# Optimization experiments

Hardware: AMD Instinct MI355X
Metric: run time of the kernel (lower is better)

Reference implementation:

```python
import jax, jax.numpy as jnp
import numpy as np

B_, L_, O_, N_, S_, U_, DEL, HID, K = 16, 128, 128, 256, 64, 32, 64, 512, 4
D_OUT = DEL + N_ * U_ + N_ * S_  # 24640


def setup_inputs() -> dict:
    key = jax.random.key(0)
    ks = jax.random.split(key, 12)
    return {
        "x": jax.random.normal(ks[0], (B_, O_ + L_, S_), jnp.float32),
        "u": jax.random.normal(ks[1], (B_, 2 * L_, U_), jnp.float32),
        "A": jax.random.normal(ks[2], (N_, 1), jnp.float32) / 20.0,
        "W0": jax.random.normal(ks[3], (HID, S_), jnp.float32) * 0.05,
        "b0": jnp.zeros((HID,), jnp.float32),
        "W1": jax.random.normal(ks[4], (N_, HID), jnp.float32) * 0.05,
        "b1": jnp.zeros((N_,), jnp.float32),
        "conv_w": jax.random.normal(ks[5], (N_ + U_, 1, K), jnp.float32) * 0.3,
        "conv_b": jnp.zeros((N_ + U_,), jnp.float32),
        "Wg": jax.random.normal(ks[6], (D_OUT, N_ + U_), jnp.float32) * 0.05,
        "bg": jnp.zeros((D_OUT,), jnp.float32),
        "Wdt": jax.random.normal(ks[7], (N_, DEL), jnp.float32) * 0.05,
        "bdt": jnp.zeros((N_,), jnp.float32),
    }


def reference(x, u, A, W0, b0, W1, b1, conv_w, conv_b, Wg, bg, Wdt, bdt):
    def proj_x(v):  # Linear -> relu -> Linear (project_x)
        return jax.nn.relu(v @ W0.T + b0) @ W1.T + b1

    u = u[:, :, :U_]
    z0 = proj_x(x[:, O_ - 1, :])                       # (B, N)

    # ---- generate_matrices ----
    x_all = proj_x(x[:, :O_ - 1, :])                   # (B, O-1, N)
    u_all = u[:, :O_ - 1, :]                           # (B, O-1, U)
    old = jax.nn.silu(jnp.concatenate([x_all, u_all], axis=2))  # (B, O-1, N+U)
    old = jnp.transpose(old, (0, 2, 1))                # (B, N+U, O-1)
    old = jax.lax.conv_general_dilated(
        old, conv_w, window_strides=(1,), padding=[(K - 1, K - 1)],
        dimension_numbers=("NCH", "OIH", "NCH"), feature_group_count=N_ + U_,
    ) + conv_b[None, :, None]
    old = old[:, :, -L_:]                              # last L timesteps
    old = jax.nn.silu(jnp.transpose(old, (0, 2, 1)))   # (B, L, N+U)
    gen = old @ Wg.T + bg                              # (B, L, delta + N*U + N*S)
    delta, Bm, Cm = jnp.split(gen, [DEL, DEL + N_ * U_], axis=-1)
    delta = jax.nn.softplus(delta @ Wdt.T + bdt)       # (B, L, N)
    Bm = Bm.reshape(B_, L_, N_, U_)
    Cm = Cm.reshape(B_, L_, N_, S_)

    # ---- discretion_matrices ----
    a = A[:, 0]
    a = -jnp.where(a > 0, a, jnp.expm1(a))             # -celu(A), alpha=1
    dA = jnp.exp(delta * a)                            # (B, L, N)
    dB = ((dA - 1.0) * (1.0 / a))[..., None] * Bm      # (B, L, N, U)

    # ---- selective_scan ----
    u0 = u[:, O_ - 1:O_ - 1 + L_, :]                   # (B, L, U)
    xt = x[:, O_:O_ + L_, :]                           # (B, L, S) targets

    def step(z, inp):
        dAi, dBi, ui, Ci, xti = inp
        z = z * dAi + jnp.einsum("bnu,bu->bn", dBi, ui)
        y = jnp.einsum("bns,bn->bs", Ci, z)
        return z, (y, jnp.mean((y - xti) ** 2))

    xs = (
        jnp.swapaxes(dA, 0, 1), jnp.swapaxes(dB, 0, 1),
        jnp.swapaxes(u0, 0, 1), jnp.swapaxes(Cm, 0, 1), jnp.swapaxes(xt, 0, 1),
    )
    _, (ys, ls) = jax.lax.scan(step, z0, xs)
    loss = jnp.sum(ls) / L_
    return loss, jax.lax.stop_gradient(ys)             # ys: (L, B, S), detached as in torch
```

## Files before the change

kernel.cpp:

```cpp
#include <hip/hip_runtime.h>
#include <math.h>

#define B_   16
#define L_   128
#define O_   128
#define N_   256
#define S_   64
#define U_   32
#define DEL_ 64
#define HID_ 512
#define CH_  288
#define M_   2048
#define KD_  288
#define CM_BASE (DEL_ + N_*U_)
#define NSLICE 32

typedef __bf16 bf16_t;
typedef bf16_t bf16x8 __attribute__((ext_vector_type(8)));
typedef float  f32x4  __attribute__((ext_vector_type(4)));

#define AS1(p) ((const __attribute__((address_space(1))) void*)(unsigned long long)(const void*)(p))
#define AS3(p) ((__attribute__((address_space(3))) void*)(unsigned int)(unsigned long long)(const void*)(p))

__device__ __forceinline__ float silu_f(float x){ return x / (1.f + expf(-x)); }
__device__ __forceinline__ float softplus_f(float x){
  return fmaxf(x, 0.f) + log1pf(expf(-fabsf(x)));
}

__device__ __forceinline__ void cvt8(const float* src, bf16_t* dst){
  float4 a = ((const float4*)src)[0];
  float4 b = ((const float4*)src)[1];
  bf16x8 o;
  o[0]=(bf16_t)a.x; o[1]=(bf16_t)a.y; o[2]=(bf16_t)a.z; o[3]=(bf16_t)a.w;
  o[4]=(bf16_t)b.x; o[5]=(bf16_t)b.y; o[6]=(bf16_t)b.z; o[7]=(bf16_t)b.w;
  *(bf16x8*)dst = o;
}

#define CVT_BLOCKS 3465
#define W0_BLOCKS  16
#define W1_BLOCKS  64
#define XB_BLOCKS  64
__global__ void k_prep(const float* __restrict__ Wg, bf16_t* __restrict__ Wgbf,
                       const float* __restrict__ W0, bf16_t* __restrict__ W0bf,
                       const float* __restrict__ W1, bf16_t* __restrict__ W1bf,
                       const float* __restrict__ x,  bf16_t* __restrict__ xbf,
                       float* __restrict__ lossa){
  if (blockIdx.x == 0 && threadIdx.x < 2) lossa[threadIdx.x] = 0.f;
  if (blockIdx.x < CVT_BLOCKS) {
    int i = blockIdx.x*256 + threadIdx.x;
    if (i >= 887040) return;
    cvt8(Wg + (size_t)i*8, Wgbf + (size_t)i*8);
  } else if (blockIdx.x < CVT_BLOCKS + W0_BLOCKS) {
    int i = (blockIdx.x - CVT_BLOCKS)*256 + threadIdx.x;
    if (i >= 4096) return;
    cvt8(W0 + (size_t)i*8, W0bf + (size_t)i*8);
  } else if (blockIdx.x < CVT_BLOCKS + W0_BLOCKS + W1_BLOCKS) {
    int i = (blockIdx.x - CVT_BLOCKS - W0_BLOCKS)*256 + threadIdx.x;
    if (i >= 16384) return;
    cvt8(W1 + (size_t)i*8, W1bf + (size_t)i*8);
  } else {
    int i = (blockIdx.x - CVT_BLOCKS - W0_BLOCKS - W1_BLOCKS)*256 + threadIdx.x;
    if (i >= 16384) return;
    int m = i >> 3, c0 = (i & 7)*8;
    int b = m >> 7, t = m & 127;
    cvt8(x + (size_t)(((b<<8)+t)<<6) + c0, xbf + (size_t)m*64 + c0);
  }
}

#define STAGE64(GBASE, ROW0G, STRIDE, LDSARR)                                        \
  { const bf16_t* gp = (GBASE) + (size_t)((ROW0G) + wave*16 + lm)*(STRIDE) + kk + lq*8; \
    __builtin_amdgcn_global_load_lds(AS1(gp), AS3(&(LDSARR)[wave*512]), 16, 0, 0); }

__global__ __launch_bounds__(256) void k_mlp1m(
    const bf16_t* __restrict__ xbf, const bf16_t* __restrict__ W0bf,
    const float* __restrict__ b0, bf16_t* __restrict__ Hbf){
  __shared__ __align__(16) bf16_t As[64*32];
  __shared__ __align__(16) bf16_t Bs[64*32];
  int tid = threadIdx.x;
  int wave = tid >> 6, lane = tid & 63;
  int wm = wave & 1, wn = wave >> 1;
  int nt = blockIdx.x, mt = blockIdx.y;
  int m0 = mt*64, n0 = nt*64;
  int lm = lane & 15, lq = lane >> 4;

  f32x4 acc[2][2];
  #pragma unroll
  for (int i=0;i<2;i++)
    #pragma unroll
    for (int j=0;j<2;j++){ acc[i][j][0]=0.f;acc[i][j][1]=0.f;acc[i][j][2]=0.f;acc[i][j][3]=0.f; }

  #pragma unroll
  for (int kk = 0; kk < 64; kk += 32) {
    STAGE64(xbf, m0, 64, As);
    STAGE64(W0bf, n0, 64, Bs);
    __syncthreads();
    bf16x8 af[2], bff[2];
    #pragma unroll
    for (int i=0;i<2;i++) af[i]  = *(const bf16x8*)&As[(wm*2 + i)*512 + lane*8];
    #pragma unroll
    for (int j=0;j<2;j++) bff[j] = *(const bf16x8*)&Bs[(wn*2 + j)*512 + lane*8];
    #pragma unroll
    for (int i=0;i<2;i++)
      #pragma unroll
      for (int j=0;j<2;j++)
        acc[i][j] = __builtin_amdgcn_mfma_f32_16x16x32_bf16(af[i], bff[j], acc[i][j], 0,0,0);
    __syncthreads();
  }
  #pragma unroll
  for (int i=0;i<2;i++)
    #pragma unroll
    for (int j=0;j<2;j++){
      int col = n0 + wn*32 + j*16 + lm;
      float bb = b0[col];
      #pragma unroll
      for (int r=0;r<4;r++){
        int row = m0 + wm*32 + i*16 + lq*4 + r;
        Hbf[(size_t)row*HID_ + col] = (bf16_t)fmaxf(acc[i][j][r] + bb, 0.f);
      }
    }
}

__global__ __launch_bounds__(256) void k_mlp2m(
    const bf16_t* __restrict__ Hbf, const bf16_t* __restrict__ W1bf,
    const float* __restrict__ b1, float* __restrict__ P){
  __shared__ __align__(16) bf16_t As[64*32];
  __shared__ __align__(16) bf16_t Bs[64*32];
  int tid = threadIdx.x;
  int wave = tid >> 6, lane = tid & 63;
  int wm = wave & 1, wn = wave >> 1;
  int nt = blockIdx.x, mt = blockIdx.y;
  int m0 = mt*64, n0 = nt*64;
  int lm = lane & 15, lq = lane >> 4;

  f32x4 acc[2][2];
  #pragma unroll
  for (int i=0;i<2;i++)
    #pragma unroll
    for (int j=0;j<2;j++){ acc[i][j][0]=0.f;acc[i][j][1]=0.f;acc[i][j][2]=0.f;acc[i][j][3]=0.f; }

  for (int kk = 0; kk < HID_; kk += 32) {
    STAGE64(Hbf, m0, HID_, As);
    STAGE64(W1bf, n0, HID_, Bs);
    __syncthreads();
    bf16x8 af[2], bff[2];
    #pragma unroll
    for (int i=0;i<2;i++) af[i]  = *(const bf16x8*)&As[(wm*2 + i)*512 + lane*8];
    #pragma unroll
    for (int j=0;j<2;j++) bff[j] = *(const bf16x8*)&Bs[(wn*2 + j)*512 + lane*8];
    #pragma unroll
    for (int i=0;i<2;i++)
      #pragma unroll
      for (int j=0;j<2;j++)
        acc[i][j] = __builtin_amdgcn_mfma_f32_16x16x32_bf16(af[i], bff[j], acc[i][j], 0,0,0);
    __syncthreads();
  }
  #pragma unroll
  for (int i=0;i<2;i++)
    #pragma unroll
    for (int j=0;j<2;j++){
      int col = n0 + wn*32 + j*16 + lm;
      float bb = b1[col];
      #pragma unroll
      for (int r=0;r<4;r++){
        int row = m0 + wm*32 + i*16 + lq*4 + r;
        P[(size_t)row*N_ + col] = acc[i][j][r] + bb;
      }
    }
}

__global__ __launch_bounds__(256) void k_convdelta(
    const float* __restrict__ P, const float* __restrict__ u,
    const float* __restrict__ cw, const float* __restrict__ cb,
    const float* __restrict__ Wg, const float* __restrict__ bg,
    const float* __restrict__ Wdt, const float* __restrict__ bdt,
    const float* __restrict__ Ap, bf16_t* __restrict__ oldbf,
    float* __restrict__ dA, float* __restrict__ coef){
  __shared__ __align__(16) float olds[4*KD_];
  __shared__ float dr[4][64];
  int tid = threadIdx.x;
  int m0 = blockIdx.x * 4;
  int b = m0 >> 7, l0 = m0 & 127;
  for (int e = tid; e < 4*CH_; e += 256) {
    int r = e / CH_, c = e - r*CH_;
    int l = l0 + r;
    float acc = cb[c];
    #pragma unroll
    for (int k = 0; k < 4; k++) {
      int t = l + k - 1;
      if (t >= 0 && t <= O_-2) {
        float s = (c < N_) ? P[((b<<7)+t)*N_ + c] : u[((b<<8)+t)*U_ + (c-N_)];
        acc += silu_f(s) * cw[c*4 + k];
      }
    }
    float v = silu_f(acc);
    olds[e] = v;
    oldbf[(size_t)(m0+r)*CH_ + c] = (bf16_t)v;
  }
  __syncthreads();
  {
    int d = tid & 63;
    int r = tid >> 6;
    const float* wrow = Wg + (size_t)d*KD_;
    const float* orow = olds + r*KD_;
    float s = 0.f;
    for (int k = 0; k < KD_; k++) s += orow[k] * wrow[k];
    dr[r][d] = s + bg[d];
  }
  __syncthreads();
  int n = tid;
  float wrow[64];
  #pragma unroll
  for (int d = 0; d < 64; d++) wrow[d] = Wdt[n*64 + d];
  float a0 = Ap[n];
  float a = -(a0 > 0.f ? a0 : expm1f(a0));
  float inva = 1.f / a;
  float bd = bdt[n];
  #pragma unroll
  for (int r = 0; r < 4; r++) {
    float s = bd;
    #pragma unroll
    for (int d = 0; d < 64; d++) s += dr[r][d] * wrow[d];
    float dd = softplus_f(s);
    float e  = expf(dd * a);
    size_t m = m0 + r;
    dA[m*N_ + n]   = e;
    coef[m*N_ + n] = (e - 1.f) * inva;
  }
}

#define STAGE_FR96(GBASE, ROW0G, LDSARR)                                                 \
  { _Pragma("unroll")                                                                    \
    for (int c = 0; c < 3; c++) {                                                        \
      _Pragma("unroll")                                                                  \
      for (int q = 0; q < 2; q++) {                                                      \
        int g = wave*2 + q;                                                              \
        const bf16_t* gp = (GBASE) + (size_t)((ROW0G) + g*16 + lm)*KD_ + kk + c*32 + lq*8;\
        __builtin_amdgcn_global_load_lds(AS1(gp), AS3(&(LDSARR)[c*4096 + g*512]), 16, 0, 0);\
      } } }

__global__ __launch_bounds__(256, 2) void k_bmfma(
    const bf16_t* __restrict__ oldbf, const bf16_t* __restrict__ Wgbf,
    const float* __restrict__ bg, const float* __restrict__ u,
    const float* __restrict__ coef, const float* __restrict__ dAg,
    const float* __restrict__ Pg, float* __restrict__ zall){
  __shared__ union {
    struct { __align__(16) bf16_t A[3*4096]; __align__(16) bf16_t B[3*4096]; } st;
    struct { float wl[128][4]; float dal[128][4]; } sc;
  } sm;
  int tid = threadIdx.x;
  int wave = tid >> 6, lane = tid & 63;
  int wm = wave & 1, wn = wave >> 1;
  int mt = blockIdx.y, nt = blockIdx.x;
  int m0 = mt*128, ncol0 = nt*128;
  int lm = lane & 15, lq = lane >> 4;

  f32x4 acc[4][4];
  #pragma unroll
  for (int i=0;i<4;i++)
    #pragma unroll
    for (int j=0;j<4;j++){ acc[i][j][0]=0.f;acc[i][j][1]=0.f;acc[i][j][2]=0.f;acc[i][j][3]=0.f; }

  for (int kk = 0; kk < KD_; kk += 96) {
    STAGE_FR96(oldbf, m0, sm.st.A);
    STAGE_FR96(Wgbf, DEL_ + ncol0, sm.st.B);
    __syncthreads();
    for (int c = 0; c < 3; c++) {
      bf16x8 af[4], bff[4];
      #pragma unroll
      for (int i=0;i<4;i++) af[i]  = *(const bf16x8*)&sm.st.A[c*4096 + (wm*4 + i)*512 + lane*8];
      #pragma unroll
      for (int j=0;j<4;j++) bff[j] = *(const bf16x8*)&sm.st.B[c*4096 + (wn*4 + j)*512 + lane*8];
      #pragma unroll
      for (int i=0;i<4;i++)
        #pragma unroll
        for (int j=0;j<4;j++)
          acc[i][j] = __builtin_amdgcn_mfma_f32_16x16x32_bf16(af[i], bff[j], acc[i][j], 0,0,0);
    }
    __syncthreads();
  }

  for (int e = tid; e < 512; e += 256)
    sm.sc.dal[e>>2][e&3] = dAg[(size_t)(m0 + (e>>2))*N_ + nt*4 + (e&3)];

  float bgv[4];
  #pragma unroll
  for (int j=0;j<4;j++) bgv[j] = bg[DEL_ + ncol0 + wn*64 + j*16 + lm];
  float p[2][4][4];
  #pragma unroll
  for (int a=0;a<2;a++)
    #pragma unroll
    for (int i=0;i<4;i++)
      #pragma unroll
      for (int r=0;r<4;r++) p[a][i][r]=0.f;
  #pragma unroll
  for (int i=0;i<4;i++){
    #pragma unroll
    for (int r=0;r<4;r++){
      int m = m0 + wm*64 + i*16 + lq*4 + r;
      int b = m >> 7, l = m & 127;
      const float* urow = u + ((size_t)(b<<8) + 127 + l)*U_;
      #pragma unroll
      for (int j=0;j<4;j++){
        float uu = urow[(j&1)*16 + lm];
        p[j>>1][i][r] += (acc[i][j][r] + bgv[j]) * uu;
      }
    }
  }
  #pragma unroll
  for (int mk = 1; mk < 16; mk <<= 1){
    #pragma unroll
    for (int a=0;a<2;a++)
      #pragma unroll
      for (int i=0;i<4;i++)
        #pragma unroll
        for (int r=0;r<4;r++) p[a][i][r] += __shfl_xor(p[a][i][r], mk);
  }
  if (lm == 0){
    #pragma unroll
    for (int nl=0;nl<2;nl++){
      int n = ((ncol0 + wn*64 + nl*32) >> 5);
      int nc = wn*2 + nl;
      #pragma unroll
      for (int i=0;i<4;i++)
        #pragma unroll
        for (int r=0;r<4;r++){
          int l = wm*64 + i*16 + lq*4 + r;
          sm.sc.wl[l][nc] = coef[(size_t)(m0+l)*N_ + n] * p[nl][i][r];
        }
    }
  }
  __syncthreads();

  {
    int nc = wave;
    int n = nt*4 + nc;
    float z0 = Pg[(size_t)(m0 + 127)*N_ + n];
    int l0 = lane*2;
    float a0 = sm.sc.dal[l0][nc],   w0 = sm.sc.wl[l0][nc];
    float a1 = sm.sc.dal[l0+1][nc], w1 = sm.sc.wl[l0+1][nc];
    float A = a0*a1, Bv = w0*a1 + w1;
    #pragma unroll
    for (int d = 1; d < 64; d <<= 1){
      float Ap = __shfl_up(A, d);
      float Bp = __shfl_up(Bv, d);
      if (lane >= d){ Bv = Bp*A + Bv; A = Ap*A; }
    }
    float Ae = __shfl_up(A, 1);
    float Be = __shfl_up(Bv, 1);
    if (lane == 0){ Ae = 1.f; Be = 0.f; }
    float zp = z0*Ae + Be;
    float za = zp*a0 + w0;
    float zb = za*a1 + w1;
    zall[(size_t)(m0 + l0)*N_ + n]     = za;
    zall[(size_t)(m0 + l0 + 1)*N_ + n] = zb;
  }
}

__global__ __launch_bounds__(256, 2) void k_cmfma(
    const bf16_t* __restrict__ oldbf, const bf16_t* __restrict__ Wgbf,
    const float* __restrict__ bg, const float* __restrict__ zall,
    float* __restrict__ ypart){
  __shared__ union {
    struct { __align__(16) bf16_t A[3*4096];
             __align__(16) bf16_t Bb[3*4096];
             float zl[128][8]; } st;
    float ylds[128][64];
  } sm;
  int tid = threadIdx.x;
  int wave = tid >> 6, lane = tid & 63;
  int wm = wave & 1, wn = wave >> 1;
  int mt = blockIdx.y, grp = blockIdx.x;
  int m0 = mt*128;
  int lm = lane & 15, lq = lane >> 4;

  for (int e = tid; e < 1024; e += 256)
    sm.st.zl[e>>3][e&7] = zall[(size_t)(m0 + (e>>3))*N_ + grp*8 + (e&7)];

  f32x4 yacc[4][4];
  #pragma unroll
  for (int i=0;i<4;i++)
    #pragma unroll
    for (int j=0;j<4;j++){ yacc[i][j][0]=0.f;yacc[i][j][1]=0.f;yacc[i][j][2]=0.f;yacc[i][j][3]=0.f; }

  for (int kh = 0; kh < 3; kh++) {
    int kk = kh*96;
    STAGE_FR96(oldbf, m0, sm.st.A);
    for (int it = 0; it < 4; it++) {
      int ncol0 = (grp*4 + it)*128;
      STAGE_FR96(Wgbf, CM_BASE + ncol0, sm.st.Bb);
      __syncthreads();
      f32x4 acc[4][4];
      #pragma unroll
      for (int i=0;i<4;i++)
        #pragma unroll
        for (int j=0;j<4;j++){ acc[i][j][0]=0.f;acc[i][j][1]=0.f;acc[i][j][2]=0.f;acc[i][j][3]=0.f; }
      for (int c = 0; c < 3; c++) {
        bf16x8 af[4], bff[4];
        #pragma unroll
        for (int i=0;i<4;i++) af[i]  = *(const bf16x8*)&sm.st.A[c*4096 + (wm*4 + i)*512 + lane*8];
        #pragma unroll
        for (int j=0;j<4;j++) bff[j] = *(const bf16x8*)&sm.st.Bb[c*4096 + (wn*4 + j)*512 + lane*8];
        #pragma unroll
        for (int i=0;i<4;i++)
          #pragma unroll
          for (int j=0;j<4;j++)
            acc[i][j] = __builtin_amdgcn_mfma_f32_16x16x32_bf16(af[i], bff[j], acc[i][j], 0,0,0);
      }
      int nl = it*2 + wn;
      float bgv[4];
      #pragma unroll
      for (int j=0;j<4;j++)
        bgv[j] = (kh == 2) ? bg[CM_BASE + ncol0 + wn*64 + j*16 + lm] : 0.f;
      #pragma unroll
      for (int i=0;i<4;i++){
        #pragma unroll
        for (int r=0;r<4;r++){
          float zv = sm.st.zl[wm*64 + i*16 + lq*4 + r][nl];
          #pragma unroll
          for (int j=0;j<4;j++)
            yacc[i][j][r] += (acc[i][j][r] + bgv[j]) * zv;
        }
      }
      __syncthreads();
    }
  }

  if (wn == 1){
    #pragma unroll
    for (int i=0;i<4;i++)
      #pragma unroll
      for (int j=0;j<4;j++)
        #pragma unroll
        for (int r=0;r<4;r++){
          int ml = wm*64 + i*16 + lq*4 + r;
          sm.ylds[ml][j*16 + lm] = yacc[i][j][r];
        }
  }
  __syncthreads();
  if (wn == 0){
    float* dst = ypart + (size_t)grp*(M_*S_);
    #pragma unroll
    for (int i=0;i<4;i++)
      #pragma unroll
      for (int j=0;j<4;j++)
        #pragma unroll
        for (int r=0;r<4;r++){
          int ml = wm*64 + i*16 + lq*4 + r;
          int s = j*16 + lm;
          dst[(size_t)(m0+ml)*S_ + s] = yacc[i][j][r] + sm.ylds[ml][s];
        }
  }
}

__global__ void k_finalize(const float* __restrict__ ypart, const float* __restrict__ x,
                           float* __restrict__ out, float* __restrict__ lossacc){
  __shared__ float red[256];
  int tid = threadIdx.x;
  float ls = 0.f;
  #pragma unroll
  for (int q = 0; q < 2; q++) {
    int e = blockIdx.x*512 + q*256 + tid;
    int m = e >> 6, s = e & 63;
    int b = m >> 7, l = m & 127;
    float yv = 0.f;
    #pragma unroll 8
    for (int g = 0; g < NSLICE; g++) yv += ypart[(size_t)g*(M_*S_) + e];
    out[1 + (size_t)((l<<4) + b)*S_ + s] = yv;
    float xv = x[((size_t)(b<<8) + 128 + l)*S_ + s];
    float d = yv - xv;
    ls += d*d;
  }
  red[tid] = ls; __syncthreads();
  for (int st = 128; st > 0; st >>= 1) {
    if (tid < st) red[tid] += red[tid+st];
    __syncthreads();
  }
  if (tid == 0) {
    atomicAdd(&lossacc[0], red[0]);
    __threadfence();
    unsigned old = atomicAdd((unsigned*)&lossacc[1], 1u);
    if (old == 255u) {
      float tot = atomicAdd(&lossacc[0], 0.f);
      out[0] = tot * (1.f / (float)(B_*S_*L_));
    }
  }
}

extern "C" void kernel_launch(void* const* d_in, const int* in_sizes, int n_in,
                              void* d_out, int out_size, void* d_ws, size_t ws_size,
                              hipStream_t stream) {
  const float* x   = (const float*)d_in[0];
  const float* u   = (const float*)d_in[1];
  const float* Ap  = (const float*)d_in[2];
  const float* W0  = (const float*)d_in[3];
  const float* b0  = (const float*)d_in[4];
  const float* W1  = (const float*)d_in[5];
  const float* b1  = (const float*)d_in[6];
  const float* cw  = (const float*)d_in[7];
  const float* cb  = (const float*)d_in[8];
  const float* Wg  = (const float*)d_in[9];
  const float* bg  = (const float*)d_in[10];
  const float* Wdt = (const float*)d_in[11];
  const float* bdt = (const float*)d_in[12];
  float* out = (float*)d_out;

  float* ws    = (float*)d_ws;
  float* zall  = ws;
  float* lossa = zall + 524288;
  bf16_t* oldbf = (bf16_t*)(lossa + 512);
  bf16_t* Wgbf  = (bf16_t*)(lossa + 512 + 294912);
  bf16_t* W0bf  = (bf16_t*)(lossa + 512 + 294912 + 3548160);
  bf16_t* W1bf  = (bf16_t*)(lossa + 512 + 294912 + 3548160 + 16384);
  bf16_t* xbf   = (bf16_t*)(lossa + 512 + 294912 + 3548160 + 16384 + 65536);
  bf16_t* Hbf   = (bf16_t*)(lossa + 512 + 294912 + 3548160 + 16384 + 65536 + 65536);
  float* R     = lossa + 512 + 294912 + 3548160 + 16384 + 65536 + 65536 + 524288;
  float* Pp    = R;
  float* dA    = Pp   + 524288;
  float* coef  = dA   + 524288;
  float* ypart = R;

  k_prep<<<CVT_BLOCKS + W0_BLOCKS + W1_BLOCKS + XB_BLOCKS, 256, 0, stream>>>(
      Wg, Wgbf, W0, W0bf, W1, W1bf, x, xbf, lossa);
  k_mlp1m<<<dim3(HID_/64, M_/64), 256, 0, stream>>>(xbf, W0bf, b0, Hbf);
  k_mlp2m<<<dim3(N_/64, M_/64), 256, 0, stream>>>(Hbf, W1bf, b1, Pp);
  k_convdelta<<<M_/4, 256, 0, stream>>>(Pp, u, cw, cb, Wg, bg, Wdt, bdt, Ap,
                                        oldbf, dA, coef);
  k_bmfma<<<dim3(64, 16), 256, 0, stream>>>(oldbf, Wgbf, bg, u, coef, dA, Pp, zall);
  k_cmfma<<<dim3(32, 16), 256, 0, stream>>>(oldbf, Wgbf, bg, zall, ypart);
  k_finalize<<<256, 256, 0, stream>>>(ypart, x, out, lossa);
}
```

Before: 208.7 us.

## Double-buffer LDS staging in MLP, B-matrix and C-matrix GEMM kernels

Converts the four MFMA GEMM kernels from single-buffered load-sync-compute loops to double-buffered LDS pipelines. The next K-slice or weight tile is issued with global_load_lds while the current one feeds the MFMAs. The goal is to hide global-memory latency behind compute and drop one barrier per iteration. It doubles the B tile buffer in k_cmfma and changes k_bmfma to 32-wide K steps, which raises LDS use and may lower occupancy or add iterations. Correctness relies on the async LDS loads finishing before the single barrier per step, which waits only on counters the compiler inserts.

```diff
diff --git a/kernel.cpp b/kernel.cpp
--- a/kernel.cpp
+++ b/kernel.cpp
@@ -67,15 +67,33 @@
   }
 }
 
-#define STAGE64(GBASE, ROW0G, STRIDE, LDSARR)                                        \
-  { const bf16_t* gp = (GBASE) + (size_t)((ROW0G) + wave*16 + lm)*(STRIDE) + kk + lq*8; \
-    __builtin_amdgcn_global_load_lds(AS1(gp), AS3(&(LDSARR)[wave*512]), 16, 0, 0); }
+#define STAGE64K(GBASE, ROW0G, STRIDE, KK, LDSP)                                     \
+  { const bf16_t* gp_ = (GBASE) + (size_t)((ROW0G) + wave*16 + lm)*(STRIDE) + (KK) + lq*8; \
+    __builtin_amdgcn_global_load_lds(AS1(gp_), AS3((LDSP) + wave*512), 16, 0, 0); }
+
+#define STAGE32(GBASE, ROW0G, KK, LDSP)                                              \
+  { _Pragma("unroll")                                                                \
+    for (int l_ = 0; l_ < 2; l_++) {                                                 \
+      int g_ = wave*2 + l_;                                                          \
+      const bf16_t* gp_ = (GBASE) + (size_t)((ROW0G) + g_*16 + lm)*KD_ + (KK) + lq*8;\
+      __builtin_amdgcn_global_load_lds(AS1(gp_), AS3((LDSP) + g_*512), 16, 0, 0);    \
+    } }
+
+#define STAGE_FR96(GBASE, ROW0G, KK, LDSP)                                           \
+  { _Pragma("unroll")                                                                \
+    for (int c_ = 0; c_ < 3; c_++) {                                                 \
+      _Pragma("unroll")                                                              \
+      for (int q_ = 0; q_ < 2; q_++) {                                               \
+        int g_ = wave*2 + q_;                                                        \
+        const bf16_t* gp_ = (GBASE) + (size_t)((ROW0G) + g_*16 + lm)*KD_ + (KK) + c_*32 + lq*8;\
+        __builtin_amdgcn_global_load_lds(AS1(gp_), AS3((LDSP) + c_*4096 + g_*512), 16, 0, 0);\
+      } } }
 
 __global__ __launch_bounds__(256) void k_mlp1m(
     const bf16_t* __restrict__ xbf, const bf16_t* __restrict__ W0bf,
     const float* __restrict__ b0, bf16_t* __restrict__ Hbf){
-  __shared__ __align__(16) bf16_t As[64*32];
-  __shared__ __align__(16) bf16_t Bs[64*32];
+  __shared__ __align__(16) bf16_t As[2][2048];
+  __shared__ __align__(16) bf16_t Bs[2][2048];
   int tid = threadIdx.x;
   int wave = tid >> 6, lane = tid & 63;
   int wm = wave & 1, wn = wave >> 1;
@@ -89,16 +107,21 @@
     #pragma unroll
     for (int j=0;j<2;j++){ acc[i][j][0]=0.f;acc[i][j][1]=0.f;acc[i][j][2]=0.f;acc[i][j][3]=0.f; }
 
-  #pragma unroll
-  for (int kk = 0; kk < 64; kk += 32) {
-    STAGE64(xbf, m0, 64, As);
-    STAGE64(W0bf, n0, 64, Bs);
-    __syncthreads();
+  STAGE64K(xbf,  m0, 64, 0, As[0]);
+  STAGE64K(W0bf, n0, 64, 0, Bs[0]);
+  __syncthreads();
+  #pragma unroll
+  for (int t = 0; t < 2; ++t) {
+    int cur = t & 1;
+    if (t < 1) {
+      STAGE64K(xbf,  m0, 64, 32, As[1]);
+      STAGE64K(W0bf, n0, 64, 32, Bs[1]);
+    }
     bf16x8 af[2], bff[2];
     #pragma unroll
-    for (int i=0;i<2;i++) af[i]  = *(const bf16x8*)&As[(wm*2 + i)*512 + lane*8];
-    #pragma unroll
-    for (int j=0;j<2;j++) bff[j] = *(const bf16x8*)&Bs[(wn*2 + j)*512 + lane*8];
+    for (int i=0;i<2;i++) af[i]  = *(const bf16x8*)&As[cur][(wm*2 + i)*512 + lane*8];
+    #pragma unroll
+    for (int j=0;j<2;j++) bff[j] = *(const bf16x8*)&Bs[cur][(wn*2 + j)*512 + lane*8];
     #pragma unroll
     for (int i=0;i<2;i++)
       #pragma unroll
@@ -123,8 +146,8 @@
 __global__ __launch_bounds__(256) void k_mlp2m(
     const bf16_t* __restrict__ Hbf, const bf16_t* __restrict__ W1bf,
     const float* __restrict__ b1, float* __restrict__ P){
-  __shared__ __align__(16) bf16_t As[64*32];
-  __shared__ __align__(16) bf16_t Bs[64*32];
+  __shared__ __align__(16) bf16_t As[2][2048];
+  __shared__ __align__(16) bf16_t Bs[2][2048];
   int tid = threadIdx.x;
   int wave = tid >> 6, lane = tid & 63;
   int wm = wave & 1, wn = wave >> 1;
@@ -138,15 +161,21 @@
     #pragma unroll
     for (int j=0;j<2;j++){ acc[i][j][0]=0.f;acc[i][j][1]=0.f;acc[i][j][2]=0.f;acc[i][j][3]=0.f; }
 
-  for (int kk = 0; kk < HID_; kk += 32) {
-    STAGE64(Hbf, m0, HID_, As);
-    STAGE64(W1bf, n0, HID_, Bs);
-    __syncthreads();
+  STAGE64K(Hbf,  m0, HID_, 0, As[0]);
+  STAGE64K(W1bf, n0, HID_, 0, Bs[0]);
+  __syncthreads();
+  for (int t = 0; t < 16; ++t) {
+    int cur = t & 1;
+    if (t < 15) {
+      int kk = (t+1)*32;
+      STAGE64K(Hbf,  m0, HID_, kk, As[cur^1]);
+      STAGE64K(W1bf, n0, HID_, kk, Bs[cur^1]);
+    }
     bf16x8 af[2], bff[2];
     #pragma unroll
-    for (int i=0;i<2;i++) af[i]  = *(const bf16x8*)&As[(wm*2 + i)*512 + lane*8];
-    #pragma unroll
-    for (int j=0;j<2;j++) bff[j] = *(const bf16x8*)&Bs[(wn*2 + j)*512 + lane*8];
+    for (int i=0;i<2;i++) af[i]  = *(const bf16x8*)&As[cur][(wm*2 + i)*512 + lane*8];
+    #pragma unroll
+    for (int j=0;j<2;j++) bff[j] = *(const bf16x8*)&Bs[cur][(wn*2 + j)*512 + lane*8];
     #pragma unroll
     for (int i=0;i<2;i++)
       #pragma unroll
@@ -228,23 +257,13 @@
   }
 }
 
-#define STAGE_FR96(GBASE, ROW0G, LDSARR)                                                 \
-  { _Pragma("unroll")                                                                    \
-    for (int c = 0; c < 3; c++) {                                                        \
-      _Pragma("unroll")                                                                  \
-      for (int q = 0; q < 2; q++) {                                                      \
-        int g = wave*2 + q;                                                              \
-        const bf16_t* gp = (GBASE) + (size_t)((ROW0G) + g*16 + lm)*KD_ + kk + c*32 + lq*8;\
-        __builtin_amdgcn_global_load_lds(AS1(gp), AS3(&(LDSARR)[c*4096 + g*512]), 16, 0, 0);\
-      } } }
-
 __global__ __launch_bounds__(256, 2) void k_bmfma(
     const bf16_t* __restrict__ oldbf, const bf16_t* __restrict__ Wgbf,
     const float* __restrict__ bg, const float* __restrict__ u,
     const float* __restrict__ coef, const float* __restrict__ dAg,
     const float* __restrict__ Pg, float* __restrict__ zall){
   __shared__ union {
-    struct { __align__(16) bf16_t A[3*4096]; __align__(16) bf16_t B[3*4096]; } st;
+    struct { __align__(16) bf16_t A[2][4096]; __align__(16) bf16_t B[2][4096]; } st;
     struct { float wl[128][4]; float dal[128][4]; } sc;
   } sm;
   int tid = threadIdx.x;
@@ -260,22 +279,26 @@
     #pragma unroll
     for (int j=0;j<4;j++){ acc[i][j][0]=0.f;acc[i][j][1]=0.f;acc[i][j][2]=0.f;acc[i][j][3]=0.f; }
 
-  for (int kk = 0; kk < KD_; kk += 96) {
-    STAGE_FR96(oldbf, m0, sm.st.A);
-    STAGE_FR96(Wgbf, DEL_ + ncol0, sm.st.B);
-    __syncthreads();
-    for (int c = 0; c < 3; c++) {
-      bf16x8 af[4], bff[4];
-      #pragma unroll
-      for (int i=0;i<4;i++) af[i]  = *(const bf16x8*)&sm.st.A[c*4096 + (wm*4 + i)*512 + lane*8];
-      #pragma unroll
-      for (int j=0;j<4;j++) bff[j] = *(const bf16x8*)&sm.st.B[c*4096 + (wn*4 + j)*512 + lane*8];
-      #pragma unroll
-      for (int i=0;i<4;i++)
-        #pragma unroll
-        for (int j=0;j<4;j++)
-          acc[i][j] = __builtin_amdgcn_mfma_f32_16x16x32_bf16(af[i], bff[j], acc[i][j], 0,0,0);
-    }
+  STAGE32(oldbf, m0, 0, sm.st.A[0]);
+  STAGE32(Wgbf, DEL_ + ncol0, 0, sm.st.B[0]);
+  __syncthreads();
+  for (int t = 0; t < 9; ++t) {
+    int cur = t & 1;
+    if (t < 8) {
+      int kk = (t+1)*32;
+      STAGE32(oldbf, m0, kk, sm.st.A[cur^1]);
+      STAGE32(Wgbf, DEL_ + ncol0, kk, sm.st.B[cur^1]);
+    }
+    bf16x8 af[4], bff[4];
+    #pragma unroll
+    for (int i=0;i<4;i++) af[i]  = *(const bf16x8*)&sm.st.A[cur][(wm*4 + i)*512 + lane*8];
+    #pragma unroll
+    for (int j=0;j<4;j++) bff[j] = *(const bf16x8*)&sm.st.B[cur][(wn*4 + j)*512 + lane*8];
+    #pragma unroll
+    for (int i=0;i<4;i++)
+      #pragma unroll
+      for (int j=0;j<4;j++)
+        acc[i][j] = __builtin_amdgcn_mfma_f32_16x16x32_bf16(af[i], bff[j], acc[i][j], 0,0,0);
     __syncthreads();
   }
 
@@ -362,7 +385,7 @@
     float* __restrict__ ypart){
   __shared__ union {
     struct { __align__(16) bf16_t A[3*4096];
-             __align__(16) bf16_t Bb[3*4096];
+             __align__(16) bf16_t Bb[2][3*4096];
              float zl[128][8]; } st;
     float ylds[128][64];
   } sm;
@@ -382,45 +405,53 @@
     #pragma unroll
     for (int j=0;j<4;j++){ yacc[i][j][0]=0.f;yacc[i][j][1]=0.f;yacc[i][j][2]=0.f;yacc[i][j][3]=0.f; }
 
-  for (int kh = 0; kh < 3; kh++) {
-    int kk = kh*96;
-    STAGE_FR96(oldbf, m0, sm.st.A);
-    for (int it = 0; it < 4; it++) {
-      int ncol0 = (grp*4 + it)*128;
-      STAGE_FR96(Wgbf, CM_BASE + ncol0, sm.st.Bb);
-      __syncthreads();
-      f32x4 acc[4][4];
+  STAGE_FR96(oldbf, m0, 0, sm.st.A);
+  STAGE_FR96(Wgbf, CM_BASE + grp*4*128, 0, sm.st.Bb[0]);
+  __syncthreads();
+
+  for (int s = 0; s < 12; ++s) {
+    int kh = s >> 2, it = s & 3, cur = s & 1;
+    if (s < 11 && it != 3) {
+      STAGE_FR96(Wgbf, CM_BASE + (grp*4 + it + 1)*128, kh*96, sm.st.Bb[cur^1]);
+    }
+    int ncol0 = (grp*4 + it)*128;
+    f32x4 acc[4][4];
+    #pragma unroll
+    for (int i=0;i<4;i++)
+      #pragma unroll
+      for (int j=0;j<4;j++){ acc[i][j][0]=0.f;acc[i][j][1]=0.f;acc[i][j][2]=0.f;acc[i][j][3]=0.f; }
+    for (int c = 0; c < 3; c++) {
+      bf16x8 af[4], bff[4];
+      #pragma unroll
+      for (int i=0;i<4;i++) af[i]  = *(const bf16x8*)&sm.st.A[c*4096 + (wm*4 + i)*512 + lane*8];
+      #pragma unroll
+      for (int j=0;j<4;j++) bff[j] = *(const bf16x8*)&sm.st.Bb[cur][c*4096 + (wn*4 + j)*512 + lane*8];
       #pragma unroll
       for (int i=0;i<4;i++)
         #pragma unroll
-        for (int j=0;j<4;j++){ acc[i][j][0]=0.f;acc[i][j][1]=0.f;acc[i][j][2]=0.f;acc[i][j][3]=0.f; }
-      for (int c = 0; c < 3; c++) {
-        bf16x8 af[4], bff[4];
+        for (int j=0;j<4;j++)
+          acc[i][j] = __builtin_amdgcn_mfma_f32_16x16x32_bf16(af[i], bff[j], acc[i][j], 0,0,0);
+    }
+    int nl = it*2 + wn;
+    float bgv[4];
+    #pragma unroll
+    for (int j=0;j<4;j++)
+      bgv[j] = (kh == 2) ? bg[CM_BASE + ncol0 + wn*64 + j*16 + lm] : 0.f;
+    #pragma unroll
+    for (int i=0;i<4;i++){
+      #pragma unroll
+      for (int r=0;r<4;r++){
+        float zv = sm.st.zl[wm*64 + i*16 + lq*4 + r][nl];
         #pragma unroll
-        for (int i=0;i<4;i++) af[i]  = *(const bf16x8*)&sm.st.A[c*4096 + (wm*4 + i)*512 + lane*8];
-        #pragma unroll
-        for (int j=0;j<4;j++) bff[j] = *(const bf16x8*)&sm.st.Bb[c*4096 + (wn*4 + j)*512 + lane*8];
-        #pragma unroll
-        for (int i=0;i<4;i++)
-          #pragma unroll
-          for (int j=0;j<4;j++)
-            acc[i][j] = __builtin_amdgcn_mfma_f32_16x16x32_bf16(af[i], bff[j], acc[i][j], 0,0,0);
+        for (int j=0;j<4;j++)
+          yacc[i][j][r] += (acc[i][j][r] + bgv[j]) * zv;
       }
-      int nl = it*2 + wn;
-      float bgv[4];
-      #pragma unroll
-      for (int j=0;j<4;j++)
-        bgv[j] = (kh == 2) ? bg[CM_BASE + ncol0 + wn*64 + j*16 + lm] : 0.f;
-      #pragma unroll
-      for (int i=0;i<4;i++){
-        #pragma unroll
-        for (int r=0;r<4;r++){
-          float zv = sm.st.zl[wm*64 + i*16 + lq*4 + r][nl];
-          #pragma unroll
-          for (int j=0;j<4;j++)
-            yacc[i][j][r] += (acc[i][j][r] + bgv[j]) * zv;
-        }
-      }
+    }
+    __syncthreads();
+    if (s < 11 && it == 3) {
+      int kk = (kh+1)*96;
+      STAGE_FR96(oldbf, m0, kk, sm.st.A);
+      STAGE_FR96(Wgbf, CM_BASE + grp*4*128, kk, sm.st.Bb[cur^1]);
       __syncthreads();
     }
   }
```

Measured after the change: 206.3 us. About the same (-1.2%).
